# Performance work log

Hardware: AMD Instinct MI355X
Metric: run time of the kernel (lower is better)

The kernel has to match this reference:

```python
import jax, jax.numpy as jnp
import numpy as np

LOG_ZERO = -40.0
LOG_EPS = 1e-10

@jax.custom_vjp
def grad_scale(x):
    return x

def _gs_fwd(x):
    return x, None

def _gs_bwd(_, g):
    return (g * 0.01,)

grad_scale.defvjp(_gs_fwd, _gs_bwd)

def to_log_space(x):
    sign_x = jnp.sign(x)
    sign_x = jnp.where(sign_x == 0, jnp.ones_like(sign_x), sign_x)
    abs_x = jnp.abs(x)
    log_x = jnp.where(abs_x > LOG_EPS, jnp.log(jnp.maximum(abs_x, LOG_EPS)), LOG_ZERO)
    return log_x, sign_x

def from_log_space(log_x, sign_x):
    mask = log_x > LOG_ZERO + 1.0
    res = sign_x * jnp.exp(jnp.minimum(grad_scale(log_x), 20.0))
    return jnp.where(mask, res, jnp.zeros_like(res))

def signed_log_add(log_a, sign_a, log_b, sign_b):
    a_is_zero = log_a <= LOG_ZERO + 1.0
    b_is_zero = log_b <= LOG_ZERO + 1.0
    max_log = jnp.maximum(log_a, log_b)
    min_log = jnp.minimum(log_a, log_b)
    diff = min_log - max_log
    a_is_max = log_a >= log_b
    sign_max = jnp.where(a_is_max, sign_a, sign_b)
    sign_min = jnp.where(a_is_max, sign_b, sign_a)
    same_sign = sign_max * sign_min > 0
    exp_diff = jnp.exp(diff)
    log_same = max_log + jnp.log1p(exp_diff)
    log_opp = max_log + jnp.log1p(-jnp.minimum(exp_diff, 0.9999))
    log_result = jnp.where(same_sign, log_same, log_opp)
    sign_result = sign_max
    log_result = jnp.where(a_is_zero, log_b, log_result)
    sign_result = jnp.where(a_is_zero, sign_b, sign_result)
    log_result = jnp.where(b_is_zero & ~a_is_zero, log_a, log_result)
    sign_result = jnp.where(b_is_zero & ~a_is_zero, sign_a, sign_result)
    return log_result, sign_result

def soft_bound_log(log_h):
    return -jax.nn.softplus(-log_h)


def setup_inputs() -> dict:
    key = jax.random.key(0)
    T, B, D = 512, 16, 1024
    k = jax.random.split(key, 4)
    xav = float(np.sqrt(6.0 / (D + D)))  # xavier_uniform bound base
    return {
        'x': jax.random.normal(k[0], (T, B, D), jnp.float32),
        'W_x': jax.random.uniform(k[1], (D, D), jnp.float32, -0.5 * xav, 0.5 * xav),
        'W_alpha': jax.random.uniform(k[2], (D, D), jnp.float32, -0.1 * xav, 0.1 * xav),
        'W_delta': jax.random.uniform(k[3], (D, D), jnp.float32, -0.1 * xav, 0.1 * xav),
        'b': jnp.zeros(D, jnp.float32),
        'b_alpha': jnp.zeros(D, jnp.float32),
        'b_delta': jnp.full((D,), -2.0, jnp.float32),
        'log_r_h': jnp.full((D,), -2.0, jnp.float32),
        'sign_r_h': jnp.ones(D, jnp.float32),
    }


def reference(x, W_x, W_alpha, W_delta, b, b_alpha, b_delta, log_r_h, sign_r_h):
    T, B, D = x.shape
    # Precompute all input projections (the compute-heavy GEMMs) in one shot.
    alpha_raw = jnp.einsum('tbd,ed->tbe', x, W_alpha) + b_alpha        # [T,B,D]
    alpha = 1.0 + jax.nn.softplus(alpha_raw)
    lin = jnp.einsum('tbd,ed->tbe', x, W_x) + b                        # [T,B,D]
    log_input, sign_input = to_log_space(lin)
    delta_raw = jnp.einsum('tbd,ed->tbe', x, W_delta) + b_delta        # [T,B,D]
    log_delta = jax.nn.log_sigmoid(delta_raw)
    log_1m_delta = jax.nn.log_sigmoid(-delta_raw)

    log_h0 = jnp.full((B, D), LOG_ZERO, x.dtype)
    sign_h0 = jnp.ones((B, D), x.dtype)

    def step(carry, inp):
        log_hp, sign_hp = carry
        a_t, log_in, sign_in, log_d, log_1md = inp
        log_rh = log_r_h + log_hp
        sign_rh = sign_r_h * sign_hp
        log_v, sign_v = signed_log_add(log_rh, sign_rh, log_in, sign_in)
        log_cand = soft_bound_log(a_t * log_v)
        log_h_new, sign_h_new = signed_log_add(log_1md + log_hp, sign_hp,
                                               log_d + log_cand, sign_v)
        h_lin = from_log_space(log_h_new, sign_h_new)
        return (log_h_new, sign_h_new), (log_h_new, sign_h_new, h_lin)

    _, (log_hs, sign_hs, h_linear) = jax.lax.scan(
        step, (log_h0, sign_h0), (alpha, log_input, sign_input, log_delta, log_1m_delta))
    log_h = jnp.concatenate([log_h0[None], log_hs], axis=0)    # [T+1,B,D]
    sign_h = jnp.concatenate([sign_h0[None], sign_hs], axis=0) # [T+1,B,D]
    return log_h, sign_h, h_linear
```

## Files before the change

### kernel.cpp

```cpp
#include <hip/hip_runtime.h>
#include <math.h>

#define BD 16384
#define TT 512
#define KDIM 1024
#define NDIM 1024
#define GEMM_M 8192
#define PANEL_Q 320
#define LOGE2F 0.69314718246459960938f

__device__ __forceinline__ float np_expf(float x)   { return expf(x); }
__device__ __forceinline__ float np_logf(float x)   { return logf(x); }
__device__ __forceinline__ float np_log1pf(float x) { return log1pf(x); }

__device__ __forceinline__ float np_softplus(float v) {
    const float e  = np_expf(-fabsf(v));
    const float l1 = np_log1pf(e);
    const float r  = __fadd_rn(fmaxf(v, 0.0f), l1);
    return (v == 0.0f) ? LOGE2F : r;
}

__device__ __forceinline__ void np_sla(float la, float sa, float lb, float sb,
                                       float& lo, float& so) {
    bool az = la <= -39.0f;
    bool bz = lb <= -39.0f;
    float mx = fmaxf(la, lb);
    float mn = fminf(la, lb);
    float diff = __fsub_rn(mn, mx);
    bool amax = la >= lb;
    float smax = amax ? sa : sb;
    float smin = amax ? sb : sa;
    bool same = __fmul_rn(smax, smin) > 0.0f;
    float ed = np_expf(diff);
    float ls  = __fadd_rn(mx, np_log1pf(ed));
    float lop = __fadd_rn(mx, np_log1pf(-fminf(ed, 0.9999f)));
    float l = same ? ls : lop;
    float s = smax;
    l = az ? lb : l;  s = az ? sb : s;
    bool bo = bz && !az;
    l = bo ? la : l;  s = bo ? sa : s;
    lo = l; so = s;
}

__global__ __launch_bounds__(256) void gemm_blas(
    const float* __restrict__ x,
    const float* __restrict__ Wa, const float* __restrict__ Wx, const float* __restrict__ Wd,
    const float* __restrict__ ba, const float* __restrict__ bx, const float* __restrict__ bd,
    float* __restrict__ out_a, float* __restrict__ out_x, float* __restrict__ out_d)
{
    const int z = blockIdx.z;
    const float* W    = (z == 0) ? Wa : (z == 1) ? Wx : Wd;
    const float* bias = (z == 0) ? ba : (z == 1) ? bx : bd;
    float* out        = (z == 0) ? out_a : (z == 1) ? out_x : out_d;

    const int m0 = blockIdx.x * 128;
    const int n0 = blockIdx.y * 128;

    __shared__ float As[16][132];
    __shared__ float Bs[16][132];

    const int tid = threadIdx.x;
    const int lr = tid >> 2;
    const int lc = tid & 3;
    const int ty = tid >> 4;
    const int tx = tid & 15;

    const float* Ap = x + (size_t)(m0 + lr) * KDIM + lc * 4;
    const float* Bp = W + (size_t)(n0 + lr) * KDIM + lc * 4;

    float4 aR0 = *(const float4*)(Ap);
    float4 aR1 = *(const float4*)(Ap + (size_t)64 * KDIM);
    float4 bR0 = *(const float4*)(Bp);
    float4 bR1 = *(const float4*)(Bp + (size_t)64 * KDIM);

    float tot[8][8];
    float acc[8][8];
    #pragma unroll
    for (int i = 0; i < 8; ++i)
        #pragma unroll
        for (int j = 0; j < 8; ++j) { tot[i][j] = 0.0f; acc[i][j] = 0.0f; }

    for (int kt = 0; kt < KDIM; kt += 16) {
        if (kt == PANEL_Q || kt == 2 * PANEL_Q || kt == 3 * PANEL_Q) {
            #pragma unroll
            for (int i = 0; i < 8; ++i)
                #pragma unroll
                for (int j = 0; j < 8; ++j) {
                    tot[i][j] = __fadd_rn(tot[i][j], acc[i][j]);
                    acc[i][j] = 0.0f;
                }
        }
        __syncthreads();
        {
            const float* a0 = (const float*)&aR0;
            const float* a1 = (const float*)&aR1;
            const float* b0 = (const float*)&bR0;
            const float* b1 = (const float*)&bR1;
            #pragma unroll
            for (int c = 0; c < 4; ++c) {
                As[lc * 4 + c][lr]      = a0[c];
                As[lc * 4 + c][lr + 64] = a1[c];
                Bs[lc * 4 + c][lr]      = b0[c];
                Bs[lc * 4 + c][lr + 64] = b1[c];
            }
        }
        __syncthreads();
        if (kt + 16 < KDIM) {
            aR0 = *(const float4*)(Ap + kt + 16);
            aR1 = *(const float4*)(Ap + (size_t)64 * KDIM + kt + 16);
            bR0 = *(const float4*)(Bp + kt + 16);
            bR1 = *(const float4*)(Bp + (size_t)64 * KDIM + kt + 16);
        }
        #pragma unroll
        for (int kk = 0; kk < 16; ++kk) {
            const float4 a0 = *(const float4*)&As[kk][ty * 8];
            const float4 a1 = *(const float4*)&As[kk][ty * 8 + 4];
            const float4 b0 = *(const float4*)&Bs[kk][tx * 8];
            const float4 b1 = *(const float4*)&Bs[kk][tx * 8 + 4];
            const float av[8] = {a0.x, a0.y, a0.z, a0.w, a1.x, a1.y, a1.z, a1.w};
            const float bv[8] = {b0.x, b0.y, b0.z, b0.w, b1.x, b1.y, b1.z, b1.w};
            #pragma unroll
            for (int i = 0; i < 8; ++i)
                #pragma unroll
                for (int j = 0; j < 8; ++j)
                    acc[i][j] = __fmaf_rn(av[i], bv[j], acc[i][j]);
        }
    }
    #pragma unroll
    for (int i = 0; i < 8; ++i)
        #pragma unroll
        for (int j = 0; j < 8; ++j)
            tot[i][j] = __fadd_rn(tot[i][j], acc[i][j]);

    float bj[8];
    #pragma unroll
    for (int j = 0; j < 8; ++j) bj[j] = bias[n0 + tx * 8 + j];

    #pragma unroll
    for (int i = 0; i < 8; ++i) {
        float* op = out + (size_t)(m0 + ty * 8 + i) * NDIM + n0 + tx * 8;
        float4 v0, v1;
        v0.x = __fadd_rn(tot[i][0], bj[0]); v0.y = __fadd_rn(tot[i][1], bj[1]);
        v0.z = __fadd_rn(tot[i][2], bj[2]); v0.w = __fadd_rn(tot[i][3], bj[3]);
        v1.x = __fadd_rn(tot[i][4], bj[4]); v1.y = __fadd_rn(tot[i][5], bj[5]);
        v1.z = __fadd_rn(tot[i][6], bj[6]); v1.w = __fadd_rn(tot[i][7], bj[7]);
        *(float4*)(op)     = v0;
        *(float4*)(op + 4) = v1;
    }
}

__device__ __forceinline__ void gl_lds(const float* g, float* l) {
    __builtin_amdgcn_global_load_lds(
        (const __attribute__((address_space(1))) void*)g,
        (__attribute__((address_space(3))) void*)l, 4, 0, 0);
}

#define WAITVM(N) do {                                                   \
    asm volatile("s_waitcnt vmcnt(" #N ")" ::: "memory");                \
    __builtin_amdgcn_sched_barrier(0); } while (0)

__global__ __launch_bounds__(192, 1) void scan_kernel(
    float* __restrict__ log_h, float* __restrict__ sign_h, float* __restrict__ h_lin,
    const float* __restrict__ log_r_h, const float* __restrict__ sign_r_h)
{
    __shared__ float Xr[4][5][4][64];
    __shared__ float Or[4][2][4][64];
    __shared__ float Rr[4][12][64];

    const int wv = threadIdx.x >> 6;
    const int ln = threadIdx.x & 63;
    const int idx = blockIdx.x * 64 + ln;

#define ISSUE_LOADS(GG, SL) do {                                         \
    const int _b = (GG) * 4;                                             \
    _Pragma("unroll")                                                    \
    for (int u = 0; u < 4; ++u) {                                        \
        gl_lds(h_lin  + (size_t)(_b + u) * BD + idx,     &Rr[SL][u * 3 + 0][0]); \
        gl_lds(log_h  + (size_t)(_b + u + 1) * BD + idx, &Rr[SL][u * 3 + 1][0]); \
        gl_lds(sign_h + (size_t)(_b + u + 1) * BD + idx, &Rr[SL][u * 3 + 2][0]); \
    } } while (0)

#define XFORM_TO(GG) do {                                                \
    const int _s = (GG) & 3;                                             \
    _Pragma("unroll")                                                    \
    for (int u = 0; u < 4; ++u) {                                        \
        const float araw = Rr[_s][u * 3 + 0][ln];                        \
        const float lin  = Rr[_s][u * 3 + 1][ln];                        \
        const float dr   = Rr[_s][u * 3 + 2][ln];                        \
        Xr[_s][0][u][ln] = __fadd_rn(1.0f, np_softplus(araw));           \
        const float ax = fabsf(lin);                                     \
        Xr[_s][1][u][ln] = (ax > 1e-10f) ? np_logf(fmaxf(ax, 1e-10f))    \
                                         : -40.0f;                       \
        Xr[_s][2][u][ln] = (lin < 0.0f) ? -1.0f : 1.0f;                  \
        const float e  = np_expf(-fabsf(dr));                            \
        const float l1 = np_log1pf(e);                                   \
        const float big = -__fadd_rn(fabsf(dr), l1);                     \
        const float sml = -l1;                                           \
        const float ld0 = (dr > 0.0f) ? sml : big;                       \
        const float lm0 = (dr > 0.0f) ? big : sml;                       \
        Xr[_s][3][u][ln] = (dr == 0.0f) ? -LOGE2F : ld0;                 \
        Xr[_s][4][u][ln] = (dr == 0.0f) ? -LOGE2F : lm0;                 \
    } } while (0)

#define WRITE_GROUP(GG) do {                                             \
    const int _s = (GG) & 3;                                             \
    _Pragma("unroll")                                                    \
    for (int u = 0; u < 4; ++u) {                                        \
        const int t = (GG) * 4 + u;                                      \
        const float lhn = Or[_s][0][u][ln];                              \
        const float shn = Or[_s][1][u][ln];                              \
        const float res = __fmul_rn(shn, np_expf(fminf(lhn, 20.0f)));    \
        const float h = (lhn > -39.0f) ? res : 0.0f;                     \
        log_h[(size_t)(t + 1) * BD + idx] = lhn;                         \
        sign_h[(size_t)(t + 1) * BD + idx] = shn;                        \
        h_lin[(size_t)t * BD + idx] = h;                                 \
    } } while (0)

    float lrh = 0.0f, srh = 0.0f;
    if (wv == 1) {
        const int d = idx & 1023;
        lrh = log_r_h[d];
        srh = sign_r_h[d];
    } else if (wv == 0) {
        ISSUE_LOADS(0, 0);
        ISSUE_LOADS(1, 1);
        WAITVM(0);
        XFORM_TO(0);
        XFORM_TO(1);
        ISSUE_LOADS(2, 2);
    } else {
        log_h[idx] = -40.0f;
        sign_h[idx] = 1.0f;
    }
    __syncthreads();

    float lhp = -40.0f, shp = 1.0f;

    for (int g = 0; g < 128; ++g) {
        if (wv == 0) {
            const int gl = (g + 3 < 128) ? g + 3 : 127;
            ISSUE_LOADS(gl, (g + 3) & 3);
            WAITVM(12);
            if (g + 2 < 128) XFORM_TO(g + 2);
        } else if (wv == 1) {
            const int s = g & 3;
            float xa[4], xli[4], xsi[4], xld[4], xlm[4];
            #pragma unroll
            for (int u = 0; u < 4; ++u) {
                xa[u]  = Xr[s][0][u][ln];
                xli[u] = Xr[s][1][u][ln];
                xsi[u] = Xr[s][2][u][ln];
                xld[u] = Xr[s][3][u][ln];
                xlm[u] = Xr[s][4][u][ln];
            }
            #pragma unroll
            for (int u = 0; u < 4; ++u) {
                const float log_rh  = __fadd_rn(lrh, lhp);
                const float sign_rh = __fmul_rn(srh, shp);
                float lv, sv;
                np_sla(log_rh, sign_rh, xli[u], xsi[u], lv, sv);
                const float tt = __fmul_rn(xa[u], lv);
                const float log_cand = -np_softplus(-tt);
                float lhn, shn;
                np_sla(__fadd_rn(xlm[u], lhp), shp,
                       __fadd_rn(xld[u], log_cand), sv, lhn, shn);
                Or[s][0][u][ln] = lhn;
                Or[s][1][u][ln] = shn;
                lhp = lhn; shp = shn;
            }
        } else {
            if (g > 0) WRITE_GROUP(g - 1);
        }
        __syncthreads();
    }
    if (wv == 2) WRITE_GROUP(127);

#undef ISSUE_LOADS
#undef XFORM_TO
#undef WRITE_GROUP
}

extern "C" void kernel_launch(void* const* d_in, const int* in_sizes, int n_in,
                              void* d_out, int out_size, void* d_ws, size_t ws_size,
                              hipStream_t stream) {
    const float* x        = (const float*)d_in[0];
    const float* W_x      = (const float*)d_in[1];
    const float* W_alpha  = (const float*)d_in[2];
    const float* W_delta  = (const float*)d_in[3];
    const float* b        = (const float*)d_in[4];
    const float* b_alpha  = (const float*)d_in[5];
    const float* b_delta  = (const float*)d_in[6];
    const float* log_r_h  = (const float*)d_in[7];
    const float* sign_r_h = (const float*)d_in[8];

    float* out    = (float*)d_out;
    float* log_h  = out;
    float* sign_h = out + (size_t)513 * BD;
    float* h_lin  = out + (size_t)2 * 513 * BD;

    dim3 ggrid(GEMM_M / 128, NDIM / 128, 3);
    gemm_blas<<<ggrid, dim3(256), 0, stream>>>(
        x, W_alpha, W_x, W_delta, b_alpha, b, b_delta,
        h_lin, log_h + BD, sign_h + BD);

    scan_kernel<<<dim3(BD / 64), dim3(192), 0, stream>>>(
        log_h, sign_h, h_lin, log_r_h, sign_r_h);
}
```

Measured before the change: 1.335 ms.

## Retile fp32 GEMM to 256x32 tiles with k-contiguous LDS layout

Replaces the 128x128 tile with 8x8 per-thread outer products by a 256x32 tile where each lane owns 4 rows and each wave 8 columns. LDS now stores A and B row-major with k contiguous, so tile stores and fragment reads are float4 without a transpose, and B reads are wave-uniform broadcasts. Occupancy is hinted at 3 blocks per CU. Separately, the signed log-add computes one log1p on a selected argument instead of two. The trade-off is less reuse per thread: 32 FMAs per 5 LDS float4 loads versus 64 per 4 before, and more global traffic for A.

```diff
diff --git a/kernel.cpp b/kernel.cpp
--- a/kernel.cpp
+++ b/kernel.cpp
@@ -8,6 +8,9 @@
 #define GEMM_M 8192
 #define PANEL_Q 320
 #define LOGE2F 0.69314718246459960938f
+#define BM 256
+#define BN 32
+#define BK 16
 
 __device__ __forceinline__ float np_expf(float x)   { return expf(x); }
 __device__ __forceinline__ float np_logf(float x)   { return logf(x); }
@@ -32,9 +35,8 @@
     float smin = amax ? sb : sa;
     bool same = __fmul_rn(smax, smin) > 0.0f;
     float ed = np_expf(diff);
-    float ls  = __fadd_rn(mx, np_log1pf(ed));
-    float lop = __fadd_rn(mx, np_log1pf(-fminf(ed, 0.9999f)));
-    float l = same ? ls : lop;
+    float arg = same ? ed : -fminf(ed, 0.9999f);
+    float l = __fadd_rn(mx, np_log1pf(arg));
     float s = smax;
     l = az ? lb : l;  s = az ? sb : s;
     bool bo = bz && !az;
@@ -42,7 +44,7 @@
     lo = l; so = s;
 }
 
-__global__ __launch_bounds__(256) void gemm_blas(
+__global__ __launch_bounds__(256, 3) void gemm_blas(
     const float* __restrict__ x,
     const float* __restrict__ Wa, const float* __restrict__ Wx, const float* __restrict__ Wd,
     const float* __restrict__ ba, const float* __restrict__ bx, const float* __restrict__ bd,
@@ -53,97 +55,95 @@
     const float* bias = (z == 0) ? ba : (z == 1) ? bx : bd;
     float* out        = (z == 0) ? out_a : (z == 1) ? out_x : out_d;
 
-    const int m0 = blockIdx.x * 128;
-    const int n0 = blockIdx.y * 128;
-
-    __shared__ float As[16][132];
-    __shared__ float Bs[16][132];
+    const int m0 = blockIdx.x * BM;
+    const int n0 = blockIdx.y * BN;
+
+    __shared__ float As[BM][20];
+    __shared__ float Bs[BN][20];
 
     const int tid = threadIdx.x;
-    const int lr = tid >> 2;
-    const int lc = tid & 3;
-    const int ty = tid >> 4;
-    const int tx = tid & 15;
-
-    const float* Ap = x + (size_t)(m0 + lr) * KDIM + lc * 4;
-    const float* Bp = W + (size_t)(n0 + lr) * KDIM + lc * 4;
-
-    float4 aR0 = *(const float4*)(Ap);
-    float4 aR1 = *(const float4*)(Ap + (size_t)64 * KDIM);
-    float4 bR0 = *(const float4*)(Bp);
-    float4 bR1 = *(const float4*)(Bp + (size_t)64 * KDIM);
-
-    float tot[8][8];
-    float acc[8][8];
-    #pragma unroll
-    for (int i = 0; i < 8; ++i)
+    const int wv  = tid >> 6;
+    const int ln  = tid & 63;
+    const int lrS = tid >> 2;
+    const int lcS = tid & 3;
+
+    const float* Ap = x + (size_t)(m0 + lrS) * KDIM + lcS * 4;
+    const float* Bp = W + (size_t)(n0 + lrS) * KDIM + lcS * 4;
+    const bool doB = (tid < 128);
+
+    float4 aS[4]; float4 bS;
+    #pragma unroll
+    for (int r = 0; r < 4; ++r)
+        aS[r] = *(const float4*)(Ap + (size_t)(64 * r) * KDIM);
+    if (doB) bS = *(const float4*)(Bp);
+
+    float tot[4][8];
+    float acc[4][8];
+    #pragma unroll
+    for (int r = 0; r < 4; ++r)
         #pragma unroll
-        for (int j = 0; j < 8; ++j) { tot[i][j] = 0.0f; acc[i][j] = 0.0f; }
-
-    for (int kt = 0; kt < KDIM; kt += 16) {
+        for (int j = 0; j < 8; ++j) { tot[r][j] = 0.0f; acc[r][j] = 0.0f; }
+
+    for (int kt = 0; kt < KDIM; kt += BK) {
         if (kt == PANEL_Q || kt == 2 * PANEL_Q || kt == 3 * PANEL_Q) {
             #pragma unroll
-            for (int i = 0; i < 8; ++i)
+            for (int r = 0; r < 4; ++r)
                 #pragma unroll
                 for (int j = 0; j < 8; ++j) {
-                    tot[i][j] = __fadd_rn(tot[i][j], acc[i][j]);
-                    acc[i][j] = 0.0f;
+                    tot[r][j] = __fadd_rn(tot[r][j], acc[r][j]);
+                    acc[r][j] = 0.0f;
                 }
         }
         __syncthreads();
-        {
-            const float* a0 = (const float*)&aR0;
-            const float* a1 = (const float*)&aR1;
-            const float* b0 = (const float*)&bR0;
-            const float* b1 = (const float*)&bR1;
-            #pragma unroll
-            for (int c = 0; c < 4; ++c) {
-                As[lc * 4 + c][lr]      = a0[c];
-                As[lc * 4 + c][lr + 64] = a1[c];
-                Bs[lc * 4 + c][lr]      = b0[c];
-                Bs[lc * 4 + c][lr + 64] = b1[c];
+        #pragma unroll
+        for (int r = 0; r < 4; ++r)
+            *(float4*)&As[lrS + 64 * r][lcS * 4] = aS[r];
+        if (doB) *(float4*)&Bs[lrS][lcS * 4] = bS;
+        __syncthreads();
+        if (kt + BK < KDIM) {
+            #pragma unroll
+            for (int r = 0; r < 4; ++r)
+                aS[r] = *(const float4*)(Ap + (size_t)(64 * r) * KDIM + kt + BK);
+            if (doB) bS = *(const float4*)(Bp + kt + BK);
+        }
+        #pragma unroll
+        for (int p = 0; p < 4; ++p) {
+            float4 Av[4];
+            #pragma unroll
+            for (int r = 0; r < 4; ++r)
+                Av[r] = *(const float4*)&As[ln + 64 * r][p * 4];
+            #pragma unroll
+            for (int j = 0; j < 8; ++j) {
+                const float4 Bv = *(const float4*)&Bs[wv * 8 + j][p * 4];
+                const float bw[4] = {Bv.x, Bv.y, Bv.z, Bv.w};
+                #pragma unroll
+                for (int kk = 0; kk < 4; ++kk) {
+                    #pragma unroll
+                    for (int r = 0; r < 4; ++r)
+                        acc[r][j] = __fmaf_rn(((const float*)&Av[r])[kk],
+                                              bw[kk], acc[r][j]);
+                }
             }
         }
-        __syncthreads();
-        if (kt + 16 < KDIM) {
-            aR0 = *(const float4*)(Ap + kt + 16);
-            aR1 = *(const float4*)(Ap + (size_t)64 * KDIM + kt + 16);
-            bR0 = *(const float4*)(Bp + kt + 16);
-            bR1 = *(const float4*)(Bp + (size_t)64 * KDIM + kt + 16);
-        }
-        #pragma unroll
-        for (int kk = 0; kk < 16; ++kk) {
-            const float4 a0 = *(const float4*)&As[kk][ty * 8];
-            const float4 a1 = *(const float4*)&As[kk][ty * 8 + 4];
-            const float4 b0 = *(const float4*)&Bs[kk][tx * 8];
-            const float4 b1 = *(const float4*)&Bs[kk][tx * 8 + 4];
-            const float av[8] = {a0.x, a0.y, a0.z, a0.w, a1.x, a1.y, a1.z, a1.w};
-            const float bv[8] = {b0.x, b0.y, b0.z, b0.w, b1.x, b1.y, b1.z, b1.w};
-            #pragma unroll
-            for (int i = 0; i < 8; ++i)
-                #pragma unroll
-                for (int j = 0; j < 8; ++j)
-                    acc[i][j] = __fmaf_rn(av[i], bv[j], acc[i][j]);
-        }
     }
     #pragma unroll
-    for (int i = 0; i < 8; ++i)
+    for (int r = 0; r < 4; ++r)
         #pragma unroll
         for (int j = 0; j < 8; ++j)
-            tot[i][j] = __fadd_rn(tot[i][j], acc[i][j]);
+            tot[r][j] = __fadd_rn(tot[r][j], acc[r][j]);
 
     float bj[8];
     #pragma unroll
-    for (int j = 0; j < 8; ++j) bj[j] = bias[n0 + tx * 8 + j];
-
-    #pragma unroll
-    for (int i = 0; i < 8; ++i) {
-        float* op = out + (size_t)(m0 + ty * 8 + i) * NDIM + n0 + tx * 8;
+    for (int j = 0; j < 8; ++j) bj[j] = bias[n0 + wv * 8 + j];
+
+    #pragma unroll
+    for (int r = 0; r < 4; ++r) {
+        float* op = out + (size_t)(m0 + ln + 64 * r) * NDIM + n0 + wv * 8;
         float4 v0, v1;
-        v0.x = __fadd_rn(tot[i][0], bj[0]); v0.y = __fadd_rn(tot[i][1], bj[1]);
-        v0.z = __fadd_rn(tot[i][2], bj[2]); v0.w = __fadd_rn(tot[i][3], bj[3]);
-        v1.x = __fadd_rn(tot[i][4], bj[4]); v1.y = __fadd_rn(tot[i][5], bj[5]);
-        v1.z = __fadd_rn(tot[i][6], bj[6]); v1.w = __fadd_rn(tot[i][7], bj[7]);
+        v0.x = __fadd_rn(tot[r][0], bj[0]); v0.y = __fadd_rn(tot[r][1], bj[1]);
+        v0.z = __fadd_rn(tot[r][2], bj[2]); v0.w = __fadd_rn(tot[r][3], bj[3]);
+        v1.x = __fadd_rn(tot[r][4], bj[4]); v1.y = __fadd_rn(tot[r][5], bj[5]);
+        v1.z = __fadd_rn(tot[r][6], bj[6]); v1.w = __fadd_rn(tot[r][7], bj[7]);
         *(float4*)(op)     = v0;
         *(float4*)(op + 4) = v1;
     }
@@ -298,7 +298,7 @@
     float* sign_h = out + (size_t)513 * BD;
     float* h_lin  = out + (size_t)2 * 513 * BD;
 
-    dim3 ggrid(GEMM_M / 128, NDIM / 128, 3);
+    dim3 ggrid(GEMM_M / BM, NDIM / BN, 3);
     gemm_blas<<<ggrid, dim3(256), 0, stream>>>(
         x, W_alpha, W_x, W_delta, b_alpha, b, b_delta,
         h_lin, log_h + BD, sign_h + BD);
```

New measurement: 1.461 ms. +9.4%, slower.
